# Optimization experiments

Hardware: AMD Instinct MI355X
Metric: run time of the kernel (lower is better)

Reference implementation:

```python
import jax, jax.numpy as jnp
import numpy as np

TOKENS = 512
IN_F = 8192
OUT_F = 8192
RANK = 64
NNZ = 8192
QMAX = 127.0  # int8 symmetric


def setup_inputs() -> dict:
    key = jax.random.key(0)
    ks = jax.random.split(key, 12)
    x = jax.random.normal(ks[0], (TOKENS, IN_F), dtype=jnp.float32)
    quantized_weight = jax.random.randint(ks[1], (OUT_F, IN_F), -128, 128, dtype=jnp.int32)
    weight_scale = jax.random.uniform(ks[2], (OUT_F,), minval=0.005, maxval=0.02, dtype=jnp.float32)
    smooth_scales = jax.random.uniform(ks[3], (IN_F,), minval=0.5, maxval=2.0, dtype=jnp.float32)
    act_scale = jnp.array([0.05], dtype=jnp.float32)
    outlier_rows = jax.random.randint(ks[4], (NNZ,), 0, OUT_F, dtype=jnp.int32)
    outlier_cols = jax.random.randint(ks[5], (NNZ,), 0, IN_F, dtype=jnp.int32)
    outlier_vals = jax.random.normal(ks[6], (NNZ,), dtype=jnp.float32) * 0.1
    svd_U = jax.random.normal(ks[7], (OUT_F, RANK), dtype=jnp.float32) * 0.02
    svd_S = jax.random.uniform(ks[8], (RANK,), minval=0.1, maxval=1.0, dtype=jnp.float32)
    svd_V = jax.random.normal(ks[9], (IN_F, RANK), dtype=jnp.float32) * 0.02
    bias = jax.random.normal(ks[10], (OUT_F,), dtype=jnp.float32) * 0.01
    return {"x": x, "quantized_weight": quantized_weight, "weight_scale": weight_scale,
            "smooth_scales": smooth_scales, "act_scale": act_scale,
            "outlier_rows": outlier_rows, "outlier_cols": outlier_cols,
            "outlier_vals": outlier_vals, "svd_U": svd_U, "svd_S": svd_S,
            "svd_V": svd_V, "bias": bias}


def reference(x, quantized_weight, weight_scale, smooth_scales, act_scale,
              outlier_rows, outlier_cols, outlier_vals, svd_U, svd_S, svd_V, bias):
    # SmoothQuant: migrate activation outliers into the weight scales
    x_s = x / smooth_scales  # [T, in]
    # per-tensor symmetric int8 activation fake-quant
    a = act_scale[0]
    x_q = jnp.clip(jnp.round(x_s / a), -QMAX - 1.0, QMAX)
    x_dq = x_q * a  # [T, in]
    # dequantize weight: per-output-channel scale, plus sparse outlier correction
    W = quantized_weight.astype(jnp.float32) * weight_scale[:, None]  # [out, in]
    W = W.at[outlier_rows, outlier_cols].add(outlier_vals)
    # dense quantized matmul
    y = x_dq @ W.T  # [T, out]
    # low-rank SVD residual: x @ (U S V^T)^T = ((x @ V) * S) @ U^T
    y = y + ((x_dq @ svd_V) * svd_S) @ svd_U.T
    return y + bias
```

## Files before the change

### kernel.cpp

```cpp
#include <hip/hip_runtime.h>
#include <hip/hip_bf16.h>

#define TOKENS 512
#define IN_F 8192
#define OUT_F 8192
#define RANK 64
#define NNZ 8192

#define KSPLIT 4
#define KRANGE (IN_F / KSPLIT)
#define BN 64
#define BK 64
#define NT (KRANGE / BK)

typedef __attribute__((ext_vector_type(8))) short short8;
typedef __attribute__((ext_vector_type(4))) float f32x4;
typedef __attribute__((ext_vector_type(4))) int int4v;

__device__ __forceinline__ unsigned short f2bf(float f) {
  unsigned int u = __builtin_bit_cast(unsigned int, f);
  u += 0x7FFFu + ((u >> 16) & 1u);
  return (unsigned short)(u >> 16);
}
__device__ __forceinline__ float bf2f(unsigned short b) {
  unsigned int u = ((unsigned int)b) << 16;
  return __builtin_bit_cast(float, u);
}

__device__ __forceinline__ void gload_lds16(const void* g, void* l) {
  __builtin_amdgcn_global_load_lds(
      (const __attribute__((address_space(1))) unsigned int*)(g),
      (__attribute__((address_space(3))) unsigned int*)(l), 16, 0, 0);
}

__global__ __launch_bounds__(256) void k_quant(const float* __restrict__ x,
                                               const float* __restrict__ smooth,
                                               const float* __restrict__ act,
                                               unsigned short* __restrict__ Abf,
                                               unsigned char* __restrict__ Aq) {
  int idx = blockIdx.x * 256 + threadIdx.x;
  int base = idx * 4;
  int col = base & (IN_F - 1);
  float a = act[0];
  float4 xx = *(const float4*)(x + base);
  float4 ss = *(const float4*)(smooth + col);
  float q0 = fminf(fmaxf(rintf((xx.x / ss.x) / a), -128.f), 127.f);
  float q1 = fminf(fmaxf(rintf((xx.y / ss.y) / a), -128.f), 127.f);
  float q2 = fminf(fmaxf(rintf((xx.z / ss.z) / a), -128.f), 127.f);
  float q3 = fminf(fmaxf(rintf((xx.w / ss.w) / a), -128.f), 127.f);
  ushort4 o;
  o.x = f2bf(q0); o.y = f2bf(q1); o.z = f2bf(q2); o.w = f2bf(q3);
  *(ushort4*)(Abf + base) = o;
  int i0 = (int)q0, i1 = (int)q1, i2 = (int)q2, i3 = (int)q3;
  unsigned int p = (i0 & 0xFF) | ((i1 & 0xFF) << 8) | ((i2 & 0xFF) << 16) |
                   ((unsigned)(i3 & 0xFF) << 24);
  *(unsigned int*)(Aq + base) = p;
}

__global__ __launch_bounds__(256) void k_lr1(const unsigned short* __restrict__ Abf,
                                             const float* __restrict__ V,
                                             const float* __restrict__ S,
                                             const float* __restrict__ act,
                                             float* __restrict__ t) {
  int bid = blockIdx.x;
  int mb = (bid & 3) * 128;
  int kb0 = (bid >> 2) * 512;
  int tid = threadIdx.x, w = tid >> 6, l = tid & 63;
  int lr = l & 15, lg = l >> 4;
  f32x4 acc[2][4] = {};
  for (int ks = 0; ks < 16; ++ks) {
    int kb = kb0 + ks * 32;
    short8 af[2];
#pragma unroll
    for (int fi = 0; fi < 2; ++fi) {
      int row = mb + w * 32 + fi * 16 + lr;
      af[fi] = *(const short8*)(Abf + (size_t)row * IN_F + kb + lg * 8);
    }
    short8 bfr[4];
#pragma unroll
    for (int fj = 0; fj < 4; ++fj) {
      int rk = fj * 16 + lr;
      short8 bv;
#pragma unroll
      for (int j = 0; j < 8; ++j)
        bv[j] = (short)f2bf(V[(size_t)(kb + lg * 8 + j) * RANK + rk]);
      bfr[fj] = bv;
    }
#pragma unroll
    for (int fi = 0; fi < 2; ++fi)
#pragma unroll
      for (int fj = 0; fj < 4; ++fj)
        acc[fi][fj] = __builtin_amdgcn_mfma_f32_16x16x32_bf16(af[fi], bfr[fj], acc[fi][fj], 0, 0, 0);
  }
  float a = act[0];
#pragma unroll
  for (int fi = 0; fi < 2; ++fi)
#pragma unroll
    for (int fj = 0; fj < 4; ++fj) {
      int rk = fj * 16 + lr;
      float sc = a * S[rk];
#pragma unroll
      for (int r = 0; r < 4; ++r) {
        int tok = mb + w * 32 + fi * 16 + lg * 4 + r;
        atomicAdd(t + tok * RANK + rk, acc[fi][fj][r] * sc);
      }
    }
}

__global__ __launch_bounds__(256) void k_lr2(const float* __restrict__ t,
                                             const float* __restrict__ U,
                                             const float* __restrict__ bias,
                                             float* __restrict__ out) {
  int bid = blockIdx.x;
  int mb = (bid & 3) * 128;
  int nb = (bid >> 2) * 128;
  int tid = threadIdx.x, w = tid >> 6, l = tid & 63;
  int lr = l & 15, lg = l >> 4;
  int wm = w >> 1, wn = w & 1;
  f32x4 acc[4][4] = {};
#pragma unroll
  for (int kk = 0; kk < 2; ++kk) {
    short8 af[4], bfr[4];
#pragma unroll
    for (int fi = 0; fi < 4; ++fi) {
      int row = mb + wm * 64 + fi * 16 + lr;
      const float4* tp = (const float4*)(t + (size_t)row * RANK + kk * 32 + lg * 8);
      float4 t0 = tp[0], t1 = tp[1];
      af[fi][0] = f2bf(t0.x); af[fi][1] = f2bf(t0.y);
      af[fi][2] = f2bf(t0.z); af[fi][3] = f2bf(t0.w);
      af[fi][4] = f2bf(t1.x); af[fi][5] = f2bf(t1.y);
      af[fi][6] = f2bf(t1.z); af[fi][7] = f2bf(t1.w);
    }
#pragma unroll
    for (int fj = 0; fj < 4; ++fj) {
      int row = nb + wn * 64 + fj * 16 + lr;
      const float4* up = (const float4*)(U + (size_t)row * RANK + kk * 32 + lg * 8);
      float4 u0 = up[0], u1 = up[1];
      bfr[fj][0] = f2bf(u0.x); bfr[fj][1] = f2bf(u0.y);
      bfr[fj][2] = f2bf(u0.z); bfr[fj][3] = f2bf(u0.w);
      bfr[fj][4] = f2bf(u1.x); bfr[fj][5] = f2bf(u1.y);
      bfr[fj][6] = f2bf(u1.z); bfr[fj][7] = f2bf(u1.w);
    }
#pragma unroll
    for (int fi = 0; fi < 4; ++fi)
#pragma unroll
      for (int fj = 0; fj < 4; ++fj)
        acc[fi][fj] = __builtin_amdgcn_mfma_f32_16x16x32_bf16(af[fi], bfr[fj], acc[fi][fj], 0, 0, 0);
  }
#pragma unroll
  for (int fj = 0; fj < 4; ++fj) {
    int o = nb + wn * 64 + fj * 16 + lr;
    float b = bias[o];
#pragma unroll
    for (int fi = 0; fi < 4; ++fi)
#pragma unroll
      for (int r = 0; r < 4; ++r) {
        int tok = mb + wm * 64 + fi * 16 + lg * 4 + r;
        out[(size_t)tok * OUT_F + o] = b + acc[fi][fj][r];
      }
  }
}

__global__ __launch_bounds__(256) void k_outlier(const unsigned short* __restrict__ Abf,
                                                 const int* __restrict__ rows,
                                                 const int* __restrict__ cols,
                                                 const float* __restrict__ vals,
                                                 const float* __restrict__ act,
                                                 float* __restrict__ out) {
  __shared__ float accr[OUT_F];
  int tk = blockIdx.x;
  for (int i = threadIdx.x; i < OUT_F; i += 256) accr[i] = 0.f;
  __syncthreads();
  float a = act[0];
  for (int i = threadIdx.x; i < NNZ; i += 256) {
    int r = rows[i], c = cols[i];
    float v = vals[i];
    float xq = bf2f(Abf[(size_t)tk * IN_F + c]);
    atomicAdd(accr + r, a * xq * v);
  }
  __syncthreads();
  float* orow = out + (size_t)tk * OUT_F;
  for (int i = threadIdx.x; i < OUT_F; i += 256) orow[i] += accr[i];
}

__global__ __launch_bounds__(512, 4) void k_gemm(const unsigned char* __restrict__ Aq,
                                                 const int* __restrict__ W,
                                                 const float* __restrict__ wscale,
                                                 const float* __restrict__ act,
                                                 float* __restrict__ out) {
  __shared__ __align__(16) unsigned char As[2][512 * BK];
  __shared__ __align__(16) unsigned char Bs[2][BN * BK];

  int d = blockIdx.x;
  int xcd = d & 7, idx = d >> 3;
  int ks = xcd >> 1;
  int nb = idx * 2 + (xcd & 1);
  int kb0 = ks * KRANGE;

  int tid = threadIdx.x, w = tid >> 6, l = tid & 63;
  int lr = l & 15, lg = l >> 4;
  int wm = w >> 1, wn = w & 1;

  int4v acc[8][2] = {};
  int4v wreg[2];

  const int rB = tid >> 3;
  const int kcB = (tid & 7) * 8;

  auto LOAD_W = [&](int kb) {
    const int* wp = W + (size_t)(nb * BN + rB) * IN_F + kb + kcB;
    wreg[0] = *(const int4v*)wp;
    wreg[1] = *(const int4v*)(wp + 4);
  };
  auto STAGE_A = [&](unsigned char* Abuf, int kb) {
#pragma unroll
    for (int i = 0; i < 4; ++i) {
      int ubase = i * 512 + w * 64;
      int ell = ubase + l;
      int r = ell >> 2, up = ell & 3;
      int u = up ^ (r & 3);
      gload_lds16(Aq + (size_t)r * IN_F + kb + u * 16, Abuf + (size_t)ubase * 16);
    }
  };
  auto WRITE_B = [&](unsigned char* Bbuf) {
    unsigned int w0 = 0, w1 = 0;
#pragma unroll
    for (int j = 0; j < 4; ++j) w0 |= ((unsigned)(wreg[0][j] & 0xFF)) << (8 * j);
#pragma unroll
    for (int j = 0; j < 4; ++j) w1 |= ((unsigned)(wreg[1][j] & 0xFF)) << (8 * j);
    int u = kcB >> 4, sub = (kcB >> 3) & 1;
    int us = u ^ (rB & 3);
    uint2 val; val.x = w0; val.y = w1;
    *(uint2*)(Bbuf + (size_t)rB * BK + us * 16 + sub * 8) = val;
  };
  auto LDF = [&](const unsigned char* buf, int row) -> int4v {
    int u = lg ^ (row & 3);
    return *(const int4v*)(buf + (size_t)row * BK + u * 16);
  };

  LOAD_W(kb0);
  STAGE_A(As[0], kb0);
  WRITE_B(Bs[0]);
  __syncthreads();

  for (int kt = 0; kt < NT; ++kt) {
    const int cur = kt & 1;
    const unsigned char* Ac = As[cur];
    const unsigned char* Bc = Bs[cur];
    if (kt + 1 < NT) {
      LOAD_W(kb0 + (kt + 1) * BK);
      STAGE_A(As[cur ^ 1], kb0 + (kt + 1) * BK);
    }
    int4v b0 = LDF(Bc, wn * 32 + lr);
    int4v b1 = LDF(Bc, wn * 32 + 16 + lr);
#pragma unroll
    for (int fi = 0; fi < 8; ++fi) {
      int4v af = LDF(Ac, wm * 128 + fi * 16 + lr);
      acc[fi][0] = __builtin_amdgcn_mfma_i32_16x16x64_i8(af, b0, acc[fi][0], 0, 0, 0);
      acc[fi][1] = __builtin_amdgcn_mfma_i32_16x16x64_i8(af, b1, acc[fi][1], 0, 0, 0);
    }
    if (kt + 1 < NT) WRITE_B(Bs[cur ^ 1]);
    __syncthreads();
  }

  float a = act[0];
#pragma unroll
  for (int fj = 0; fj < 2; ++fj) {
    int o = nb * BN + wn * 32 + fj * 16 + lr;
    float sc = a * wscale[o];
#pragma unroll
    for (int fi = 0; fi < 8; ++fi)
#pragma unroll
      for (int rr = 0; rr < 4; ++rr) {
        int tok = wm * 128 + fi * 16 + lg * 4 + rr;
        atomicAdd(out + (size_t)tok * OUT_F + o, (float)acc[fi][fj][rr] * sc);
      }
  }
}

extern "C" void kernel_launch(void* const* d_in, const int* in_sizes, int n_in,
                              void* d_out, int out_size, void* d_ws, size_t ws_size,
                              hipStream_t stream) {
  const float* x = (const float*)d_in[0];
  const int* W = (const int*)d_in[1];
  const float* wscale = (const float*)d_in[2];
  const float* smooth = (const float*)d_in[3];
  const float* act = (const float*)d_in[4];
  const int* orow = (const int*)d_in[5];
  const int* ocol = (const int*)d_in[6];
  const float* oval = (const float*)d_in[7];
  const float* U = (const float*)d_in[8];
  const float* S = (const float*)d_in[9];
  const float* V = (const float*)d_in[10];
  const float* bias = (const float*)d_in[11];
  float* out = (float*)d_out;

  unsigned short* Abf = (unsigned short*)d_ws;
  unsigned char* Aq = (unsigned char*)d_ws + (size_t)TOKENS * IN_F * 2;
  float* t = (float*)((char*)d_ws + (size_t)TOKENS * IN_F * 3);

  hipMemsetAsync(t, 0, TOKENS * RANK * sizeof(float), stream);
  k_quant<<<(TOKENS * IN_F / 4) / 256, 256, 0, stream>>>(x, smooth, act, Abf, Aq);
  k_lr1<<<64, 256, 0, stream>>>(Abf, V, S, act, t);
  k_lr2<<<256, 256, 0, stream>>>(t, U, bias, out);
  k_outlier<<<TOKENS, 256, 0, stream>>>(Abf, orow, ocol, oval, act, out);
  k_gemm<<<512, 512, 0, stream>>>(Aq, W, wscale, act, out);
}
```

Measured before the change: 187.6 us.

## Deepen gemm prefetch pipeline with manual waitcnts and split-K partials for low-rank

The int8 GEMM main loop now prefetches W two tiles ahead using two register sets. It replaces __syncthreads with explicit vmcnt/lgkmcnt waits plus a raw barrier, raises wave priority around the MFMA block, and changes the LDS XOR swizzle to use row>>1. The low-rank first stage drops from 64 to 16 blocks, each handling a larger K range. Each block writes per-split partials instead of using atomics, so the memset goes away and lr2 sums the four partials. The aim is to hide W global-load latency and remove atomic and memset overhead, at the cost of fragile hand-counted waitcnts and less parallelism in k_lr1.

```diff
diff --git a/kernel.cpp b/kernel.cpp
--- a/kernel.cpp
+++ b/kernel.cpp
@@ -32,6 +32,9 @@
       (const __attribute__((address_space(1))) unsigned int*)(g),
       (__attribute__((address_space(3))) unsigned int*)(l), 16, 0, 0);
 }
+
+#define WAIT_VM(n) asm volatile("s_waitcnt vmcnt(" #n ")" ::: "memory")
+#define WAIT_LGKM0 asm volatile("s_waitcnt lgkmcnt(0)" ::: "memory")
 
 __global__ __launch_bounds__(256) void k_quant(const float* __restrict__ x,
                                                const float* __restrict__ smooth,
@@ -64,11 +67,12 @@
                                              float* __restrict__ t) {
   int bid = blockIdx.x;
   int mb = (bid & 3) * 128;
-  int kb0 = (bid >> 2) * 512;
+  int ksp = bid >> 2;
+  int kb0 = ksp * KRANGE;
   int tid = threadIdx.x, w = tid >> 6, l = tid & 63;
   int lr = l & 15, lg = l >> 4;
   f32x4 acc[2][4] = {};
-  for (int ks = 0; ks < 16; ++ks) {
+  for (int ks = 0; ks < KRANGE / 32; ++ks) {
     int kb = kb0 + ks * 32;
     short8 af[2];
 #pragma unroll
@@ -93,6 +97,7 @@
         acc[fi][fj] = __builtin_amdgcn_mfma_f32_16x16x32_bf16(af[fi], bfr[fj], acc[fi][fj], 0, 0, 0);
   }
   float a = act[0];
+  float* tk = t + (size_t)ksp * TOKENS * RANK;
 #pragma unroll
   for (int fi = 0; fi < 2; ++fi)
 #pragma unroll
@@ -102,7 +107,7 @@
 #pragma unroll
       for (int r = 0; r < 4; ++r) {
         int tok = mb + w * 32 + fi * 16 + lg * 4 + r;
-        atomicAdd(t + tok * RANK + rk, acc[fi][fj][r] * sc);
+        tk[(size_t)tok * RANK + rk] = acc[fi][fj][r] * sc;
       }
     }
 }
@@ -124,8 +129,15 @@
 #pragma unroll
     for (int fi = 0; fi < 4; ++fi) {
       int row = mb + wm * 64 + fi * 16 + lr;
-      const float4* tp = (const float4*)(t + (size_t)row * RANK + kk * 32 + lg * 8);
-      float4 t0 = tp[0], t1 = tp[1];
+      size_t off = (size_t)row * RANK + kk * 32 + lg * 8;
+      float4 t0 = {0, 0, 0, 0}, t1 = {0, 0, 0, 0};
+#pragma unroll
+      for (int s = 0; s < KSPLIT; ++s) {
+        const float4* tp = (const float4*)(t + (size_t)s * TOKENS * RANK + off);
+        float4 u0 = tp[0], u1 = tp[1];
+        t0.x += u0.x; t0.y += u0.y; t0.z += u0.z; t0.w += u0.w;
+        t1.x += u1.x; t1.y += u1.y; t1.z += u1.z; t1.w += u1.w;
+      }
       af[fi][0] = f2bf(t0.x); af[fi][1] = f2bf(t0.y);
       af[fi][2] = f2bf(t0.z); af[fi][3] = f2bf(t0.w);
       af[fi][4] = f2bf(t1.x); af[fi][5] = f2bf(t1.y);
@@ -202,66 +214,84 @@
   int wm = w >> 1, wn = w & 1;
 
   int4v acc[8][2] = {};
-  int4v wreg[2];
+  int4v wa[2], wb[2];
 
   const int rB = tid >> 3;
   const int kcB = (tid & 7) * 8;
 
-  auto LOAD_W = [&](int kb) {
+  auto LOAD_W = [&](int4v (&wr)[2], int kb) {
     const int* wp = W + (size_t)(nb * BN + rB) * IN_F + kb + kcB;
-    wreg[0] = *(const int4v*)wp;
-    wreg[1] = *(const int4v*)(wp + 4);
-  };
-  auto STAGE_A = [&](unsigned char* Abuf, int kb) {
+    wr[0] = *(const int4v*)wp;
+    wr[1] = *(const int4v*)(wp + 4);
+  };
+  auto STAGE_A = [&](int buf, int kb) {
 #pragma unroll
     for (int i = 0; i < 4; ++i) {
       int ubase = i * 512 + w * 64;
       int ell = ubase + l;
       int r = ell >> 2, up = ell & 3;
-      int u = up ^ (r & 3);
-      gload_lds16(Aq + (size_t)r * IN_F + kb + u * 16, Abuf + (size_t)ubase * 16);
-    }
-  };
-  auto WRITE_B = [&](unsigned char* Bbuf) {
+      int u = up ^ ((r >> 1) & 3);
+      gload_lds16(Aq + (size_t)r * IN_F + kb + u * 16, &As[buf][(size_t)ubase * 16]);
+    }
+  };
+  auto WRITE_B = [&](int buf, const int4v (&wr)[2]) {
     unsigned int w0 = 0, w1 = 0;
 #pragma unroll
-    for (int j = 0; j < 4; ++j) w0 |= ((unsigned)(wreg[0][j] & 0xFF)) << (8 * j);
-#pragma unroll
-    for (int j = 0; j < 4; ++j) w1 |= ((unsigned)(wreg[1][j] & 0xFF)) << (8 * j);
+    for (int j = 0; j < 4; ++j) w0 |= ((unsigned)(wr[0][j] & 0xFF)) << (8 * j);
+#pragma unroll
+    for (int j = 0; j < 4; ++j) w1 |= ((unsigned)(wr[1][j] & 0xFF)) << (8 * j);
     int u = kcB >> 4, sub = (kcB >> 3) & 1;
-    int us = u ^ (rB & 3);
+    int us = u ^ ((rB >> 1) & 3);
     uint2 val; val.x = w0; val.y = w1;
-    *(uint2*)(Bbuf + (size_t)rB * BK + us * 16 + sub * 8) = val;
-  };
-  auto LDF = [&](const unsigned char* buf, int row) -> int4v {
-    int u = lg ^ (row & 3);
-    return *(const int4v*)(buf + (size_t)row * BK + u * 16);
-  };
-
-  LOAD_W(kb0);
-  STAGE_A(As[0], kb0);
-  WRITE_B(Bs[0]);
-  __syncthreads();
-
-  for (int kt = 0; kt < NT; ++kt) {
-    const int cur = kt & 1;
-    const unsigned char* Ac = As[cur];
-    const unsigned char* Bc = Bs[cur];
-    if (kt + 1 < NT) {
-      LOAD_W(kb0 + (kt + 1) * BK);
-      STAGE_A(As[cur ^ 1], kb0 + (kt + 1) * BK);
-    }
-    int4v b0 = LDF(Bc, wn * 32 + lr);
-    int4v b1 = LDF(Bc, wn * 32 + 16 + lr);
+    *(uint2*)(&Bs[buf][(size_t)rB * BK + us * 16 + sub * 8]) = val;
+  };
+  auto LDFA = [&](int buf, int row) -> int4v {
+    int u = lg ^ ((row >> 1) & 3);
+    return *(const int4v*)(&As[buf][(size_t)row * BK + u * 16]);
+  };
+  auto LDFB = [&](int buf, int row) -> int4v {
+    int u = lg ^ ((row >> 1) & 3);
+    return *(const int4v*)(&Bs[buf][(size_t)row * BK + u * 16]);
+  };
+  auto COMPUTE = [&](int buf) {
+    __builtin_amdgcn_s_setprio(1);
+    int4v b0 = LDFB(buf, wn * 32 + lr);
+    int4v b1 = LDFB(buf, wn * 32 + 16 + lr);
 #pragma unroll
     for (int fi = 0; fi < 8; ++fi) {
-      int4v af = LDF(Ac, wm * 128 + fi * 16 + lr);
+      int4v af = LDFA(buf, wm * 128 + fi * 16 + lr);
       acc[fi][0] = __builtin_amdgcn_mfma_i32_16x16x64_i8(af, b0, acc[fi][0], 0, 0, 0);
       acc[fi][1] = __builtin_amdgcn_mfma_i32_16x16x64_i8(af, b1, acc[fi][1], 0, 0, 0);
     }
-    if (kt + 1 < NT) WRITE_B(Bs[cur ^ 1]);
-    __syncthreads();
-  }
+    __builtin_amdgcn_s_setprio(0);
+  };
+
+  LOAD_W(wa, kb0);
+  STAGE_A(0, kb0);
+  WAIT_VM(4);
+  WRITE_B(0, wa);
+  LOAD_W(wa, kb0 + BK);
+  WAIT_VM(2);
+  WAIT_LGKM0;
+  __builtin_amdgcn_s_barrier();
+
+#define ITER(kt, CUR, wcur, wnxt)                                   \
+  {                                                                 \
+    STAGE_A(CUR ^ 1, kb0 + (((kt) + 1) & (NT - 1)) * BK);           \
+    LOAD_W(wnxt, kb0 + (((kt) + 2) & (NT - 1)) * BK);               \
+    COMPUTE(CUR);                                                   \
+    WAIT_VM(6);                                                     \
+    WRITE_B(CUR ^ 1, wcur);                                         \
+    WAIT_VM(2);                                                     \
+    WAIT_LGKM0;                                                     \
+    __builtin_amdgcn_s_barrier();                                   \
+  }
+
+  for (int kt = 0; kt < NT; kt += 2) {
+    ITER(kt, 0, wa, wb);
+    ITER(kt + 1, 1, wb, wa);
+  }
+#undef ITER
 
   float a = act[0];
 #pragma unroll
@@ -299,9 +329,8 @@
   unsigned char* Aq = (unsigned char*)d_ws + (size_t)TOKENS * IN_F * 2;
   float* t = (float*)((char*)d_ws + (size_t)TOKENS * IN_F * 3);
 
-  hipMemsetAsync(t, 0, TOKENS * RANK * sizeof(float), stream);
   k_quant<<<(TOKENS * IN_F / 4) / 256, 256, 0, stream>>>(x, smooth, act, Abf, Aq);
-  k_lr1<<<64, 256, 0, stream>>>(Abf, V, S, act, t);
+  k_lr1<<<16, 256, 0, stream>>>(Abf, V, S, act, t);
   k_lr2<<<256, 256, 0, stream>>>(t, U, bias, out);
   k_outlier<<<TOKENS, 256, 0, stream>>>(Abf, orow, ocol, oval, act, out);
   k_gemm<<<512, 512, 0, stream>>>(Aq, W, wscale, act, out);
```

New measurement: 217.2 us. +15.8%, slower.
